# Optimization experiments

Hardware: AMD Instinct MI355X
Metric: run time of the kernel (lower is better)

Reference implementation:

```python
import jax, jax.numpy as jnp
import numpy as np
from jax import lax

EXP = 3          # exp_size
TOPK = 9         # top_number
DS = 4           # down_sample (stride & kernel of conv_down)
UP = 4           # up_sample
C_CH = 64        # c
BN_EPS = 1e-5


def conv2d(x, w, b, stride, pad):
    y = lax.conv_general_dilated(x, w, (stride, stride), ((pad, pad), (pad, pad)),
                                 dimension_numbers=('NCHW', 'OIHW', 'NCHW'))
    return y + b[None, :, None, None]


def bnorm(x, g, b, m, v):
    scale = g / jnp.sqrt(v + BN_EPS)
    return (x - m[None, :, None, None]) * scale[None, :, None, None] + b[None, :, None, None]


def get_feat(x1, H, W):
    # x1: [B, C, L] flattened downsampled features
    B, C, L = x1.shape
    win = 2 * EXP + 1
    xt = jnp.transpose(x1, (0, 2, 1))                      # [B, L, C]
    # euclidean distance -> similarity 1/(1+d)
    sq = jnp.sum(xt * xt, axis=-1)                         # [B, L]
    d2 = sq[:, :, None] + sq[:, None, :] - 2.0 * jnp.einsum('blc,bmc->blm', xt, xt)
    dist = jnp.sqrt(jnp.maximum(d2, 1e-12))
    sim = 1.0 / (1.0 + dist)                               # [B, L, L]
    pad = jnp.pad(sim.reshape(B, L, H, W),
                  ((0, 0), (0, 0), (EXP, EXP), (EXP, EXP)),
                  constant_values=1e20)                    # [B, L, H+2e, W+2e]
    l = jnp.arange(L)
    row, col = l // W, l % W
    d = jnp.arange(win)
    off_i = jnp.repeat(d, win)
    off_j = jnp.tile(d, win)
    ii = row[:, None] + off_i[None, :]                     # [L, P] padded coords
    jj = col[:, None] + off_j[None, :]
    win_val = pad[:, l[:, None], ii, jj]                   # [B, L, P]
    # topk SMALLEST similarity (most dissimilar); padded 1e20 never selected
    _, idx = lax.top_k(-win_val, TOPK)                     # [B, L, k]
    h_bias = idx // win - EXP
    w_bias = idx % win - EXP
    Hf = row[None, :, None] + h_bias
    Wf = col[None, :, None] + w_bias
    index = Hf * W + Wf                                    # [B, L, k] in [0, L)
    b_idx = jnp.arange(B)[:, None, None]
    x_final = xt[b_idx, index]                             # [B, L, k, C]
    return x_final


def setup_inputs() -> dict:
    key = jax.random.key(0)
    ks = jax.random.split(key, 6)
    c = C_CH
    f32 = jnp.float32
    x = jax.random.normal(ks[0], (4, c, 256, 256), f32)
    wd = jax.random.normal(ks[1], (c, c, DS, DS), f32) * 0.05
    bd = jnp.zeros((c,), f32)
    w1 = jax.random.normal(ks[2], (c, 2 * c, 3, 3), f32) * 0.05
    b1 = jnp.zeros((c,), f32)
    wa = jax.random.normal(ks[3], (c, c, 1, 1), f32) * 0.05
    ones, zeros = jnp.ones((c,), f32), jnp.zeros((c,), f32)
    return dict(x=x,
                wd=wd, bd=bd, bnd_g=ones, bnd_b=zeros, bnd_m=zeros, bnd_v=ones,
                w1=w1, b1=b1, bn1_g=ones, bn1_b=zeros, bn1_m=zeros, bn1_v=ones,
                wa=wa, bna_g=ones, bna_b=zeros, bna_m=zeros, bna_v=ones)


def reference(x, wd, bd, bnd_g, bnd_b, bnd_m, bnd_v,
              w1, b1, bn1_g, bn1_b, bn1_m, bn1_v,
              wa, bna_g, bna_b, bna_m, bna_v):
    # conv_down: Conv(k=DS, s=DS, p=0) + BN + ReLU
    x1 = jax.nn.relu(bnorm(conv2d(x, wd, bd, DS, 0), bnd_g, bnd_b, bnd_m, bnd_v))
    B, C, H, W = x1.shape
    L = H * W
    xf = x1.reshape(B, C, L)
    x_final = get_feat(xf, H, W)                           # [B, L, k, C]
    xt = jnp.transpose(xf, (0, 2, 1))                      # [B, L, C]
    out = jnp.mean(x_final - xt[:, :, None, :], axis=2)    # [B, L, C]
    out_img = jnp.transpose(out, (0, 2, 1)).reshape(B, C, H, W)
    cat = jnp.concatenate([x1, out_img], axis=1)           # [B, 2C, H, W]
    # SENet: conv3x3 + BN + ReLU, global-avg-pool attention
    feat = jax.nn.relu(bnorm(conv2d(cat, w1, b1, 1, 1), bn1_g, bn1_b, bn1_m, bn1_v))
    att = jnp.mean(feat, axis=(2, 3), keepdims=True)       # [B, C, 1, 1]
    att = lax.conv_general_dilated(att, wa, (1, 1), ((0, 0), (0, 0)),
                                   dimension_numbers=('NCHW', 'OIHW', 'NCHW'))
    att = jax.nn.sigmoid(bnorm(att, bna_g, bna_b, bna_m, bna_v))
    out = feat * att
    # F.interpolate bilinear, align_corners=False == half-pixel resize
    return jax.image.resize(out, (B, C, H * UP, W * UP), method='bilinear')
```

## Files before the change

### kernel.cpp

```cpp
#include <hip/hip_runtime.h>
#include <hip/hip_bf16.h>
#include <stdint.h>

__device__ __forceinline__ float* catp(float* o, int p) {
    return o + (size_t)(p & 255) * 65536 + 4096 + ((p >> 8) << 12);
}
__device__ __forceinline__ double* x1hp(float* o, int q) {
    return (double*)(o + (size_t)q * 65536 + 16384);
}
__device__ __forceinline__ float wtv(const float* o, int kk, int co) {
    return o[(size_t)(kk >> 3) * 65536 + 25600 + (kk & 7) * 64 + co];
}
__device__ __forceinline__ double* wd64p(float* o, int k) {
    return (double*)(o + (size_t)(k >> 2) * 65536 + 26624) + (k & 3) * 64;
}

__global__ __launch_bounds__(256) void k0_wtrans(const float* __restrict__ w1, const float* __restrict__ wd,
                                                 float* __restrict__ o) {
    int idx = blockIdx.x * 256 + threadIdx.x;
    if (idx < 73728) {
        int co = idx & 63, kk = idx >> 6;
        o[(size_t)(kk >> 3) * 65536 + 25600 + (kk & 7) * 64 + co] = w1[co * 1152 + kk];
    } else if (idx < 139264) {
        int j = idx - 73728;
        int co = j & 63, k = j >> 6;
        wd64p(o, k)[co] = (double)wd[co * 1024 + k];
    }
}

__global__ __launch_bounds__(256) void k1_convds(
    const float* __restrict__ x, const float* __restrict__ bd,
    const float* __restrict__ g, const float* __restrict__ be,
    const float* __restrict__ m, const float* __restrict__ v,
    float* __restrict__ o)
{
    __shared__ __align__(16) double wlds[32 * 64];
    __shared__ __align__(16) double xlds[32 * 32];
    int blk = blockIdx.x;
    int jh = blk & 1, i = (blk >> 1) & 63, b = blk >> 7;
    int t = threadIdx.x;
    int tj = t & 15, tc = t >> 4;
    double acc[4][2];
    #pragma unroll
    for (int c = 0; c < 4; ++c) { acc[c][0] = 0.0; acc[c][1] = 0.0; }
    for (int p = 0; p < 32; ++p) {
        __syncthreads();
        #pragma unroll
        for (int u = 0; u < 8; ++u) {
            int idx = t + u * 256;
            int kl = idx >> 6, co = idx & 63;
            wlds[kl * 64 + co] = wd64p(o, p * 32 + kl)[co];
        }
        {
            int f4j = t & 31, ky = (t >> 5) & 3, ciL = t >> 7;
            const float* src = x + (((size_t)(b * 64 + p * 2 + ciL) * 256 + (i * 4 + ky)) * 256 + jh * 128 + f4j * 4);
            float4 f = *(const float4*)src;
            int kq = (ciL * 16 + ky * 4) * 32 + f4j;
            xlds[kq]      = (double)f.x;
            xlds[kq + 32] = (double)f.y;
            xlds[kq + 64] = (double)f.z;
            xlds[kq + 96] = (double)f.w;
        }
        __syncthreads();
        #pragma unroll
        for (int ciL = 0; ciL < 2; ++ciL) {
            #pragma unroll
            for (int ky = 0; ky < 4; ++ky) {
                int kq = ciL * 16 + ky * 4;
                double w_[4][4], x_[4][2];
                #pragma unroll
                for (int kx = 0; kx < 4; ++kx) {
                    const double* wp = wlds + (kq + kx) * 64;
                    const double* xp = xlds + (kq + kx) * 32;
                    double2 wa0 = *(const double2*)(wp + tc * 2);
                    double2 wa1 = *(const double2*)(wp + tc * 2 + 32);
                    double2 xa0 = *(const double2*)(xp + tj * 2);
                    w_[kx][0] = wa0.x; w_[kx][1] = wa0.y; w_[kx][2] = wa1.x; w_[kx][3] = wa1.y;
                    x_[kx][0] = xa0.x; x_[kx][1] = xa0.y;
                }
                #pragma unroll
                for (int c = 0; c < 4; ++c)
                    #pragma unroll
                    for (int jj = 0; jj < 2; ++jj)
                        acc[c][jj] = fma(w_[0][c], x_[0][jj],
                                     fma(w_[1][c], x_[1][jj],
                                     fma(w_[2][c], x_[2][jj],
                                     fma(w_[3][c], x_[3][jj], acc[c][jj]))));
            }
        }
    }
    #pragma unroll
    for (int c = 0; c < 4; ++c) {
        int co = ((c >> 1) << 5) + tc * 2 + (c & 1);
        double sc = (double)g[co] / sqrt((double)v[co] + 1e-5);
        double sh = (double)bd[co] - (double)m[co];
        double bb = (double)be[co];
        double o0v = fmax(0.0, (acc[c][0] + sh) * sc + bb);
        double o1v = fmax(0.0, (acc[c][1] + sh) * sc + bb);
        int pos0 = i * 64 + jh * 32 + tj * 2;
        float* cp = catp(o, b * 128 + co);
        *(float2*)(cp + pos0) = make_float2((float)o0v, (float)o1v);
        double* xh = x1hp(o, b * 64 + co);
        *(double2*)(xh + pos0) = make_double2(o0v, o1v);
    }
}

__global__ __launch_bounds__(512) void k2_feat(float* __restrict__ o)
{
    __shared__ __align__(16) char smem[29568];
    __shared__ double sqd[7 * 64];
    __shared__ int sels[64 * 9];
    double* tile_d = (double*)smem;
    double* d2s = (double*)smem;
    float* tileq = (float*)smem;
    int blk = blockIdx.x;
    int b = blk >> 6, i = blk & 63;
    int t = threadIdx.x;
    int lane = t & 63, wv = t >> 6;

    double dacc[7];
    #pragma unroll
    for (int k = 0; k < 7; ++k) dacc[k] = 0.0;
    double sq_own = 0.0;

    for (int q = 0; q < 8; ++q) {
        __syncthreads();
        for (int s = t; s < 1792; s += 512) {
            int rc = s >> 5, c2 = s & 31;
            int r = rc >> 3, c = rc & 7;
            int gr = i - 3 + r;
            if (gr >= 0 && gr <= 63) {
                const double* src = x1hp(o, b * 64 + q * 8 + c);
                *(double2*)(tile_d + rc * 66 + c2 * 2) = *(const double2*)(src + gr * 64 + c2 * 2);
            }
        }
        __syncthreads();
        if (t < 448) {
            int r = t >> 6, col = t & 63;
            int gr = i - 3 + r;
            if (gr >= 0 && gr <= 63) {
                double s = 0.0;
                #pragma unroll
                for (int c = 0; c < 8; ++c) {
                    double xv = tile_d[(r * 8 + c) * 66 + col];
                    s = fma(xv, xv, s);
                }
                sq_own += s;
            }
        }
        double xlq[8];
        #pragma unroll
        for (int c = 0; c < 8; ++c) xlq[c] = tile_d[(24 + c) * 66 + lane];
        #pragma unroll
        for (int k = 0; k < 7; ++k) {
            int oo = wv + 8 * k;
            if (oo < 49) {
                int oi = oo / 7 - 3, oj = oo % 7 - 3;
                int mi = i + oi, mj = lane + oj;
                if (mi >= 0 && mi <= 63 && mj >= 0 && mj <= 63) {
                    int r = oi + 3;
                    double dot = 0.0;
                    #pragma unroll
                    for (int c = 0; c < 8; ++c) dot = fma(xlq[c], tile_d[(r * 8 + c) * 66 + mj], dot);
                    dacc[k] += dot;
                }
            }
        }
    }
    __syncthreads();
    if (t < 448) sqd[t] = sq_own;
    __syncthreads();
    #pragma unroll
    for (int k = 0; k < 7; ++k) {
        int oo = wv + 8 * k;
        if (oo < 49) {
            int oi = oo / 7 - 3, oj = oo % 7 - 3;
            int mi = i + oi, mj = lane + oj;
            double d2 = -1e300;
            if (mi >= 0 && mi <= 63 && mj >= 0 && mj <= 63)
                d2 = sqd[192 + lane] + sqd[(oi + 3) * 64 + mj] - 2.0 * dacc[k];
            d2s[lane * 50 + oo] = d2;
        }
    }
    __syncthreads();
    if (wv == 0) {
        unsigned long long mask = 0ull;
        for (int k = 0; k < 9; ++k) {
            double best = -1e308; int bi = 0;
            for (int oo = 0; oo < 49; ++oo) {
                if ((mask >> oo) & 1ull) continue;
                double vv = d2s[lane * 50 + oo];
                if (vv > best) { best = vv; bi = oo; }
            }
            mask |= (1ull << bi);
            sels[lane * 9 + k] = bi;
        }
    }
    __syncthreads();
    int rk[9], cj[9];
    #pragma unroll
    for (int k = 0; k < 9; ++k) {
        int oo = sels[lane * 9 + k];
        rk[k] = oo / 7;
        cj[k] = lane + (oo % 7) - 3;
    }
    for (int q = 0; q < 8; ++q) {
        __syncthreads();
        for (int s = t; s < 896; s += 512) {
            int rc = s >> 4, x4 = s & 15;
            int r = rc >> 3, c = rc & 7;
            int gr = i - 3 + r;
            if (gr >= 0 && gr <= 63)
                *(float4*)(tileq + rc * 68 + x4 * 4) =
                    *(const float4*)(catp(o, b * 128 + q * 8 + c) + gr * 64 + x4 * 4);
        }
        __syncthreads();
        {
            int c = wv;
            float s = 0.f;
            #pragma unroll
            for (int k = 0; k < 9; ++k) s += tileq[(rk[k] * 8 + c) * 68 + cj[k]];
            float outv = s * (1.f / 9.f) - tileq[(24 + c) * 68 + lane];
            catp(o, b * 128 + 64 + q * 8 + c)[i * 64 + lane] = outv;
        }
    }
}

__global__ __launch_bounds__(1024) void k3_conv(
    float* __restrict__ o, const float* __restrict__ b1,
    const float* __restrict__ g, const float* __restrict__ be,
    const float* __restrict__ m, const float* __restrict__ v)
{
    __shared__ __align__(16) float wlds[16 * 9 * 64];
    __shared__ __align__(16) float xlds[3 * 16 * 72];
    int blk = blockIdx.x;
    int b = blk >> 6, i = blk & 63;
    int t = threadIdx.x;
    int co = t & 63, jg = t >> 6;
    float acc0 = 0.f, acc1 = 0.f, acc2 = 0.f, acc3 = 0.f;
    const float4 z4 = make_float4(0.f, 0.f, 0.f, 0.f);
    for (int st = 0; st < 8; ++st) {
        __syncthreads();
        for (int idx = t; idx < 9216; idx += 1024) {
            int kk = st * 144 + (idx >> 6);
            wlds[idx] = wtv(o, kk, idx & 63);
        }
        for (int f = t; f < 864; f += 1024) {
            int x4 = f % 18, rc = f / 18;
            int ry = rc >> 4, cl = rc & 15;
            int gr = i - 1 + ry;
            float4 val = z4;
            if (x4 >= 1 && x4 <= 16 && gr >= 0 && gr <= 63)
                val = *(const float4*)(catp(o, b * 128 + st * 16 + cl) + gr * 64 + (x4 - 1) * 4);
            *(float4*)(xlds + rc * 72 + x4 * 4) = val;
        }
        __syncthreads();
        for (int cl = 0; cl < 16; ++cl) {
            #pragma unroll
            for (int ry = 0; ry < 3; ++ry) {
                float w0  = wlds[(cl * 9 + ry * 3 + 0) * 64 + co];
                float w1f = wlds[(cl * 9 + ry * 3 + 1) * 64 + co];
                float w2  = wlds[(cl * 9 + ry * 3 + 2) * 64 + co];
                const float* xr = xlds + (ry * 16 + cl) * 72 + jg * 4;
                float4 q0 = *(const float4*)(xr);
                float4 q1 = *(const float4*)(xr + 4);
                float4 q2 = *(const float4*)(xr + 8);
                float xv[12] = { q0.x,q0.y,q0.z,q0.w, q1.x,q1.y,q1.z,q1.w, q2.x,q2.y,q2.z,q2.w };
                acc0 = fmaf(w0, xv[3], fmaf(w1f, xv[4], fmaf(w2, xv[5], acc0)));
                acc1 = fmaf(w0, xv[4], fmaf(w1f, xv[5], fmaf(w2, xv[6], acc1)));
                acc2 = fmaf(w0, xv[5], fmaf(w1f, xv[6], fmaf(w2, xv[7], acc2)));
                acc3 = fmaf(w0, xv[6], fmaf(w1f, xv[7], fmaf(w2, xv[8], acc3)));
            }
        }
    }
    float sc = g[co] * rsqrtf(v[co] + 1e-5f);
    float sh = b1[co] - m[co];
    float bb = be[co];
    float4 ov;
    ov.x = fmaxf(0.f, fmaf(acc0 + sh, sc, bb));
    ov.y = fmaxf(0.f, fmaf(acc1 + sh, sc, bb));
    ov.z = fmaxf(0.f, fmaf(acc2 + sh, sc, bb));
    ov.w = fmaxf(0.f, fmaf(acc3 + sh, sc, bb));
    *(float4*)(o + (size_t)(b * 64 + co) * 65536 + i * 64 + jg * 4) = ov;
}

__global__ __launch_bounds__(256) void k4_mean(float* __restrict__ o) {
    int q = blockIdx.x, t = threadIdx.x;
    const float* p = o + (size_t)q * 65536;
    float s = 0.f;
    for (int k = t; k < 4096; k += 256) s += p[k];
    #pragma unroll
    for (int off = 32; off > 0; off >>= 1) s += __shfl_down(s, off, 64);
    __shared__ float red[4];
    if ((t & 63) == 0) red[t >> 6] = s;
    __syncthreads();
    if (t == 0) o[(size_t)q * 65536 + 12288] = (red[0] + red[1] + red[2] + red[3]) * (1.f / 4096.f);
}

__global__ __launch_bounds__(256) void k4_att(float* __restrict__ o, const float* __restrict__ wa,
    const float* __restrict__ g, const float* __restrict__ be, const float* __restrict__ m, const float* __restrict__ v) {
    int t = threadIdx.x;
    int b = t >> 6, co = t & 63;
    const float* wr = wa + co * 64;
    float s = 0.f;
    for (int ci = 0; ci < 64; ++ci) s = fmaf(wr[ci], o[(size_t)(b * 64 + ci) * 65536 + 12288], s);
    float sc = g[co] * rsqrtf(v[co] + 1e-5f);
    float y = fmaf(s - m[co], sc, be[co]);
    o[(size_t)t * 65536 + 12289] = 1.f / (1.f + expf(-y));
}

__global__ __launch_bounds__(1024) void k5_up(float* __restrict__ o) {
    __shared__ __align__(16) float fplane[4096];
    int bc = blockIdx.x;
    int t = threadIdx.x;
    float* slot = o + (size_t)bc * 65536;
    *(float4*)(fplane + t * 4) = *(const float4*)(slot + t * 4);
    float att = slot[12289];
    __syncthreads();
    int ox = t & 255, oyc = t >> 8;
    float fx = ox * 0.25f - 0.375f;
    int ix = (int)floorf(fx);
    float wx = fx - (float)ix;
    int x0 = ix < 0 ? 0 : ix;
    int x1 = (ix + 1 > 63) ? 63 : ix + 1;
    for (int oy = oyc * 64; oy < oyc * 64 + 64; ++oy) {
        float fy = oy * 0.25f - 0.375f;
        int iy = (int)floorf(fy);
        float wy = fy - (float)iy;
        int y0 = iy < 0 ? 0 : iy;
        int y1 = (iy + 1 > 63) ? 63 : iy + 1;
        float a  = fplane[y0 * 64 + x0], b_ = fplane[y0 * 64 + x1];
        float c_ = fplane[y1 * 64 + x0], d_ = fplane[y1 * 64 + x1];
        float top = a + wx * (b_ - a);
        float bot = c_ + wx * (d_ - c_);
        float val = (top + wy * (bot - top)) * att;
        slot[oy * 256 + ox] = val;
    }
}

extern "C" void kernel_launch(void* const* d_in, const int* in_sizes, int n_in,
                              void* d_out, int out_size, void* d_ws, size_t ws_size,
                              hipStream_t stream) {
    const float* x     = (const float*)d_in[0];
    const float* wd    = (const float*)d_in[1];
    const float* bd    = (const float*)d_in[2];
    const float* bnd_g = (const float*)d_in[3];
    const float* bnd_b = (const float*)d_in[4];
    const float* bnd_m = (const float*)d_in[5];
    const float* bnd_v = (const float*)d_in[6];
    const float* w1    = (const float*)d_in[7];
    const float* b1    = (const float*)d_in[8];
    const float* bn1_g = (const float*)d_in[9];
    const float* bn1_b = (const float*)d_in[10];
    const float* bn1_m = (const float*)d_in[11];
    const float* bn1_v = (const float*)d_in[12];
    const float* wa    = (const float*)d_in[13];
    const float* bna_g = (const float*)d_in[14];
    const float* bna_b = (const float*)d_in[15];
    const float* bna_m = (const float*)d_in[16];
    const float* bna_v = (const float*)d_in[17];

    float* o = (float*)d_out;

    hipLaunchKernelGGL(k0_wtrans, dim3(544), dim3(256), 0, stream, w1, wd, o);
    hipLaunchKernelGGL(k1_convds, dim3(512), dim3(256), 0, stream,
                       x, bd, bnd_g, bnd_b, bnd_m, bnd_v, o);
    hipLaunchKernelGGL(k2_feat, dim3(256), dim3(512), 0, stream, o);
    hipLaunchKernelGGL(k3_conv, dim3(256), dim3(1024), 0, stream,
                       o, b1, bn1_g, bn1_b, bn1_m, bn1_v);
    hipLaunchKernelGGL(k4_mean, dim3(256), dim3(256), 0, stream, o);
    hipLaunchKernelGGL(k4_att, dim3(1), dim3(256), 0, stream,
                       o, wa, bna_g, bna_b, bna_m, bna_v);
    hipLaunchKernelGGL(k5_up, dim3(256), dim3(1024), 0, stream, o);
}
```

Measured before the change: 240.4 us.

## Double-buffer LDS tiles in downsample conv with register prefetch

Result: no change. 240.3 us (-0.1%).

```diff
diff --git a/kernel.cpp b/kernel.cpp
--- a/kernel.cpp
+++ b/kernel.cpp
@@ -34,34 +34,50 @@
     const float* __restrict__ m, const float* __restrict__ v,
     float* __restrict__ o)
 {
-    __shared__ __align__(16) double wlds[32 * 64];
-    __shared__ __align__(16) double xlds[32 * 32];
+    __shared__ __align__(16) double wlds[2][32 * 64];
+    __shared__ __align__(16) double xlds[2][32 * 32];
     int blk = blockIdx.x;
     int jh = blk & 1, i = (blk >> 1) & 63, b = blk >> 7;
     int t = threadIdx.x;
     int tj = t & 15, tc = t >> 4;
+    int s_f4j = t & 31, s_ky = (t >> 5) & 3, s_ciL = t >> 7;
+    int s_kq = (s_ciL * 16 + s_ky * 4) * 32 + s_f4j;
+
     double acc[4][2];
     #pragma unroll
     for (int c = 0; c < 4; ++c) { acc[c][0] = 0.0; acc[c][1] = 0.0; }
+
+    double wreg[8];
+    float4 xreg;
+    #pragma unroll
+    for (int u = 0; u < 8; ++u) {
+        int idx = t + u * 256;
+        wreg[u] = wd64p(o, (idx >> 6))[idx & 63];
+    }
+    xreg = *(const float4*)(x + (((size_t)(b * 64 + s_ciL) * 256 + (i * 4 + s_ky)) * 256 + jh * 128 + s_f4j * 4));
+    #pragma unroll
+    for (int u = 0; u < 8; ++u) {
+        int idx = t + u * 256;
+        wlds[0][(idx >> 6) * 64 + (idx & 63)] = wreg[u];
+    }
+    xlds[0][s_kq]      = (double)xreg.x;
+    xlds[0][s_kq + 32] = (double)xreg.y;
+    xlds[0][s_kq + 64] = (double)xreg.z;
+    xlds[0][s_kq + 96] = (double)xreg.w;
+    __syncthreads();
+
     for (int p = 0; p < 32; ++p) {
-        __syncthreads();
-        #pragma unroll
-        for (int u = 0; u < 8; ++u) {
-            int idx = t + u * 256;
-            int kl = idx >> 6, co = idx & 63;
-            wlds[kl * 64 + co] = wd64p(o, p * 32 + kl)[co];
-        }
-        {
-            int f4j = t & 31, ky = (t >> 5) & 3, ciL = t >> 7;
-            const float* src = x + (((size_t)(b * 64 + p * 2 + ciL) * 256 + (i * 4 + ky)) * 256 + jh * 128 + f4j * 4);
-            float4 f = *(const float4*)src;
-            int kq = (ciL * 16 + ky * 4) * 32 + f4j;
-            xlds[kq]      = (double)f.x;
-            xlds[kq + 32] = (double)f.y;
-            xlds[kq + 64] = (double)f.z;
-            xlds[kq + 96] = (double)f.w;
-        }
-        __syncthreads();
+        int cur = p & 1;
+        if (p + 1 < 32) {
+            #pragma unroll
+            for (int u = 0; u < 8; ++u) {
+                int idx = t + u * 256;
+                wreg[u] = wd64p(o, (p + 1) * 32 + (idx >> 6))[idx & 63];
+            }
+            xreg = *(const float4*)(x + (((size_t)(b * 64 + (p + 1) * 2 + s_ciL) * 256 + (i * 4 + s_ky)) * 256 + jh * 128 + s_f4j * 4));
+        }
+        const double* wb = wlds[cur];
+        const double* xb = xlds[cur];
         #pragma unroll
         for (int ciL = 0; ciL < 2; ++ciL) {
             #pragma unroll
@@ -70,8 +86,8 @@
                 double w_[4][4], x_[4][2];
                 #pragma unroll
                 for (int kx = 0; kx < 4; ++kx) {
-                    const double* wp = wlds + (kq + kx) * 64;
-                    const double* xp = xlds + (kq + kx) * 32;
+                    const double* wp = wb + (kq + kx) * 64;
+                    const double* xp = xb + (kq + kx) * 32;
                     double2 wa0 = *(const double2*)(wp + tc * 2);
                     double2 wa1 = *(const double2*)(wp + tc * 2 + 32);
                     double2 xa0 = *(const double2*)(xp + tj * 2);
@@ -87,6 +103,19 @@
                                      fma(w_[2][c], x_[2][jj],
                                      fma(w_[3][c], x_[3][jj], acc[c][jj]))));
             }
+        }
+        if (p + 1 < 32) {
+            int nxt = (p + 1) & 1;
+            #pragma unroll
+            for (int u = 0; u < 8; ++u) {
+                int idx = t + u * 256;
+                wlds[nxt][(idx >> 6) * 64 + (idx & 63)] = wreg[u];
+            }
+            xlds[nxt][s_kq]      = (double)xreg.x;
+            xlds[nxt][s_kq + 32] = (double)xreg.y;
+            xlds[nxt][s_kq + 64] = (double)xreg.z;
+            xlds[nxt][s_kq + 96] = (double)xreg.w;
+            __syncthreads();
         }
     }
     #pragma unroll
```
